# Kernel optimization log

Measured on AMD Instinct MI355X. Metric: run time of the kernel, lower is better.

## Reference

```python
import jax, jax.numpy as jnp
import numpy as np

N_NODES = 100000
N_EDGES = 640000
D = 128
L = 3
NUM_GRAPHS = 128


def setup_inputs() -> dict:
    key = jax.random.key(0)
    ks = jax.random.split(key, 8)
    scale = 1.0 / np.sqrt(D)
    x = jax.random.normal(ks[0], (N_NODES, D), dtype=jnp.float32)
    edge_index = jax.random.randint(ks[1], (2, N_EDGES), 0, N_NODES, dtype=jnp.int64)
    batch = jnp.sort(jax.random.randint(ks[2], (N_NODES,), 0, NUM_GRAPHS, dtype=jnp.int64))
    W1 = jax.random.normal(ks[3], (L, D, D), dtype=jnp.float32) * scale
    b1 = jnp.zeros((L, D), dtype=jnp.float32)
    W2 = jax.random.normal(ks[4], (L, D, D), dtype=jnp.float32) * scale
    b2 = jnp.zeros((L, D), dtype=jnp.float32)
    return {"x": x, "edge_index": edge_index, "batch": batch,
            "W1": W1, "b1": b1, "W2": W2, "b2": b2}


def reference(x, edge_index, batch, W1, b1, W2, b2):
    # GIN forward: per layer z = ReLU(MLP((1+eps)*z + sum_{j in N(i)} z_j)), eps=0
    n = x.shape[0]
    src, dst = edge_index[0], edge_index[1]  # messages flow src -> dst
    z = x
    for l in range(W1.shape[0]):
        agg = jax.ops.segment_sum(z[src], dst, num_segments=n)  # scatter-add aggregation
        h = agg + z                                             # (1+eps)*x_i + sum x_j, eps=0
        h = jnp.maximum(h @ W1[l] + b1[l], 0.0)                 # Linear + ReLU
        z = h @ W2[l] + b2[l]                                   # Linear
        z = jnp.maximum(z, 0.0)                                 # F.relu after conv
    # global mean pool over graph ids (dropout is identity in eval / p=0)
    ones = jnp.ones((n,), dtype=z.dtype)
    counts = jax.ops.segment_sum(ones, batch, num_segments=NUM_GRAPHS)
    sums = jax.ops.segment_sum(z, batch, num_segments=NUM_GRAPHS)
    g = sums / jnp.maximum(counts, 1.0)[:, None]
    return z, g
```

## Files before the change

### kernel.cpp

```cpp
#include <hip/hip_runtime.h>
#include <hip/hip_bf16.h>

#define D 128
#define NG 128

typedef __attribute__((ext_vector_type(8))) short bf16x8;
typedef __attribute__((ext_vector_type(4))) float f32x4;

__device__ inline unsigned short f2bf(float f) {
  union { float f; unsigned u; } c; c.f = f;
  unsigned u = c.u;
  return (unsigned short)((u + 0x7FFFu + ((u >> 16) & 1u)) >> 16);
}
__device__ inline float bf2f(unsigned short b) {
  union { unsigned u; float f; } c; c.u = ((unsigned)b) << 16;
  return c.f;
}

__global__ void prep_w(const float* __restrict__ W1, const float* __restrict__ W2,
                       unsigned short* __restrict__ Wt1, unsigned short* __restrict__ Wt2,
                       int* __restrict__ deg, int N, float* __restrict__ g) {
  int t = blockIdx.x * 256 + threadIdx.x;
  if (t < N) deg[t] = 0;
  if (t < NG * D) g[t] = 0.f;
  if (t >= 3 * 128 * 128) return;
  int l = t >> 14, k = (t >> 7) & 127, n = t & 127;
  int o = (l << 14) + (n << 7) + k;
  Wt1[o] = f2bf(W1[t]);
  Wt2[o] = f2bf(W2[t]);
}


__global__ void hist_deg(const int* __restrict__ dst, int* __restrict__ deg, int E) {
  int e = blockIdx.x * 256 + threadIdx.x;
  if (e < E) atomicAdd(deg + dst[e], 1);
}

__global__ __launch_bounds__(256) void scan1(const int* __restrict__ deg,
    int* __restrict__ rowptr, int* __restrict__ bsum, int n) {
  __shared__ int sh[256];
  int tid = threadIdx.x;
  int idx = blockIdx.x * 1024 + tid * 4;
  int v[4], tsum = 0;
#pragma unroll
  for (int j = 0; j < 4; ++j) { v[j] = (idx + j < n) ? deg[idx + j] : 0; tsum += v[j]; }
  sh[tid] = tsum;
  __syncthreads();
  for (int off = 1; off < 256; off <<= 1) {
    int x = (tid >= off) ? sh[tid - off] : 0;
    __syncthreads();
    sh[tid] += x;
    __syncthreads();
  }
  if (tid == 255) bsum[blockIdx.x] = sh[255];
  int run = sh[tid] - tsum;
#pragma unroll
  for (int j = 0; j < 4; ++j) { if (idx + j < n) rowptr[idx + j] = run; run += v[j]; }
}

__global__ __launch_bounds__(128) void scan2(int* __restrict__ bsum, int nb) {
  __shared__ int sh[128];
  int tid = threadIdx.x;
  int v = (tid < nb) ? bsum[tid] : 0;
  sh[tid] = v;
  __syncthreads();
  for (int off = 1; off < 128; off <<= 1) {
    int x = (tid >= off) ? sh[tid - off] : 0;
    __syncthreads();
    sh[tid] += x;
    __syncthreads();
  }
  if (tid < nb) bsum[tid] = sh[tid] - v;
}

__global__ void scan3(int* __restrict__ rowptr, int* __restrict__ pos,
                      const int* __restrict__ bsum, int n, int E) {
  int t = blockIdx.x * 256 + threadIdx.x;
  if (t < n) {
    int v = rowptr[t] + bsum[t >> 10];
    rowptr[t] = v;
    pos[t] = v;
  }
  if (t == 0) rowptr[n] = E;
}

__global__ void edge_scatter(const int* __restrict__ src, const int* __restrict__ dst,
                             int* __restrict__ pos, int* __restrict__ csr_src, int E) {
  int e = blockIdx.x * 256 + threadIdx.x;
  if (e >= E) return;
  int idx = atomicAdd(pos + dst[e], 1);
  csr_src[idx] = src[e];
}


template<bool IN_BF16>
__global__ __launch_bounds__(256) void gather_agg(const void* __restrict__ zin,
    const int* __restrict__ rowptr, const int* __restrict__ csr_src,
    unsigned short* __restrict__ agg, int N) {
  int t = blockIdx.x * 256 + threadIdx.x;
  int node = t >> 3;
  if (node >= N) return;
  int c = (t & 7) * 16;
  const float* zf = (const float*)zin;
  const unsigned short* zb = (const unsigned short*)zin;

  float acc[16];

  if constexpr (IN_BF16) {
    const unsigned short* p = zb + (size_t)node * D + c;
    bf16x8 v0 = *(const bf16x8*)(p);
    bf16x8 v1 = *(const bf16x8*)(p + 8);
#pragma unroll
    for (int j = 0; j < 8; ++j) {
      acc[j]     = bf2f((unsigned short)v0[j]);
      acc[j + 8] = bf2f((unsigned short)v1[j]);
    }
  } else {
    const float* p = zf + (size_t)node * D + c;
    float4 v0 = *(const float4*)(p);
    float4 v1 = *(const float4*)(p + 4);
    float4 v2 = *(const float4*)(p + 8);
    float4 v3 = *(const float4*)(p + 12);
    acc[0]  = v0.x; acc[1]  = v0.y; acc[2]  = v0.z; acc[3]  = v0.w;
    acc[4]  = v1.x; acc[5]  = v1.y; acc[6]  = v1.z; acc[7]  = v1.w;
    acc[8]  = v2.x; acc[9]  = v2.y; acc[10] = v2.z; acc[11] = v2.w;
    acc[12] = v3.x; acc[13] = v3.y; acc[14] = v3.z; acc[15] = v3.w;
  }

  int e  = rowptr[node];
  int e1 = rowptr[node + 1];

  if constexpr (IN_BF16) {
    for (; e + 4 <= e1; e += 4) {
      int s0 = csr_src[e + 0];
      int s1 = csr_src[e + 1];
      int s2 = csr_src[e + 2];
      int s3 = csr_src[e + 3];
      const unsigned short* p0 = zb + (size_t)s0 * D + c;
      const unsigned short* p1 = zb + (size_t)s1 * D + c;
      const unsigned short* p2 = zb + (size_t)s2 * D + c;
      const unsigned short* p3 = zb + (size_t)s3 * D + c;
      bf16x8 a0 = *(const bf16x8*)(p0), a1 = *(const bf16x8*)(p0 + 8);
      bf16x8 b0 = *(const bf16x8*)(p1), b1 = *(const bf16x8*)(p1 + 8);
      bf16x8 c0 = *(const bf16x8*)(p2), c1 = *(const bf16x8*)(p2 + 8);
      bf16x8 d0 = *(const bf16x8*)(p3), d1 = *(const bf16x8*)(p3 + 8);
#pragma unroll
      for (int j = 0; j < 8; ++j) {
        acc[j]     += (bf2f((unsigned short)a0[j]) + bf2f((unsigned short)b0[j]))
                    + (bf2f((unsigned short)c0[j]) + bf2f((unsigned short)d0[j]));
        acc[j + 8] += (bf2f((unsigned short)a1[j]) + bf2f((unsigned short)b1[j]))
                    + (bf2f((unsigned short)c1[j]) + bf2f((unsigned short)d1[j]));
      }
    }
    if (e + 2 <= e1) {
      int s0 = csr_src[e + 0];
      int s1 = csr_src[e + 1];
      const unsigned short* p0 = zb + (size_t)s0 * D + c;
      const unsigned short* p1 = zb + (size_t)s1 * D + c;
      bf16x8 a0 = *(const bf16x8*)(p0), a1 = *(const bf16x8*)(p0 + 8);
      bf16x8 b0 = *(const bf16x8*)(p1), b1 = *(const bf16x8*)(p1 + 8);
#pragma unroll
      for (int j = 0; j < 8; ++j) {
        acc[j]     += bf2f((unsigned short)a0[j]) + bf2f((unsigned short)b0[j]);
        acc[j + 8] += bf2f((unsigned short)a1[j]) + bf2f((unsigned short)b1[j]);
      }
      e += 2;
    }
    if (e < e1) {
      int s0 = csr_src[e];
      const unsigned short* p0 = zb + (size_t)s0 * D + c;
      bf16x8 a0 = *(const bf16x8*)(p0), a1 = *(const bf16x8*)(p0 + 8);
#pragma unroll
      for (int j = 0; j < 8; ++j) {
        acc[j]     += bf2f((unsigned short)a0[j]);
        acc[j + 8] += bf2f((unsigned short)a1[j]);
      }
    }
  } else {
    for (; e + 2 <= e1; e += 2) {
      int s0 = csr_src[e + 0];
      int s1 = csr_src[e + 1];
      const float* p0 = zf + (size_t)s0 * D + c;
      const float* p1 = zf + (size_t)s1 * D + c;
      float4 u0 = *(const float4*)(p0);
      float4 u1 = *(const float4*)(p0 + 4);
      float4 u2 = *(const float4*)(p0 + 8);
      float4 u3 = *(const float4*)(p0 + 12);
      float4 w0 = *(const float4*)(p1);
      float4 w1 = *(const float4*)(p1 + 4);
      float4 w2 = *(const float4*)(p1 + 8);
      float4 w3 = *(const float4*)(p1 + 12);
      acc[0]  += u0.x + w0.x; acc[1]  += u0.y + w0.y;
      acc[2]  += u0.z + w0.z; acc[3]  += u0.w + w0.w;
      acc[4]  += u1.x + w1.x; acc[5]  += u1.y + w1.y;
      acc[6]  += u1.z + w1.z; acc[7]  += u1.w + w1.w;
      acc[8]  += u2.x + w2.x; acc[9]  += u2.y + w2.y;
      acc[10] += u2.z + w2.z; acc[11] += u2.w + w2.w;
      acc[12] += u3.x + w3.x; acc[13] += u3.y + w3.y;
      acc[14] += u3.z + w3.z; acc[15] += u3.w + w3.w;
    }
    if (e < e1) {
      int s0 = csr_src[e];
      const float* p0 = zf + (size_t)s0 * D + c;
      float4 u0 = *(const float4*)(p0);
      float4 u1 = *(const float4*)(p0 + 4);
      float4 u2 = *(const float4*)(p0 + 8);
      float4 u3 = *(const float4*)(p0 + 12);
      acc[0]  += u0.x; acc[1]  += u0.y; acc[2]  += u0.z; acc[3]  += u0.w;
      acc[4]  += u1.x; acc[5]  += u1.y; acc[6]  += u1.z; acc[7]  += u1.w;
      acc[8]  += u2.x; acc[9]  += u2.y; acc[10] += u2.z; acc[11] += u2.w;
      acc[12] += u3.x; acc[13] += u3.y; acc[14] += u3.z; acc[15] += u3.w;
    }
  }

  bf16x8 o0, o1;
#pragma unroll
  for (int j = 0; j < 8; ++j) {
    o0[j] = (short)f2bf(acc[j]);
    o1[j] = (short)f2bf(acc[j + 8]);
  }
  unsigned short* q = agg + (size_t)node * D + c;
  *(bf16x8*)(q)     = o0;
  *(bf16x8*)(q + 8) = o1;
}


template<bool LAST>
__global__ __launch_bounds__(256, 2) void gemm_fused(const unsigned short* __restrict__ A,
    const unsigned short* __restrict__ Wt1, const float* __restrict__ b1v,
    const unsigned short* __restrict__ Wt2, const float* __restrict__ b2v,
    unsigned short* __restrict__ Zb, float* __restrict__ Zf, int M, int nt) {
  __shared__ unsigned short w2s[128][136];
  __shared__ unsigned short hs[4][16][136];
  int tid  = threadIdx.x;
  int lane = tid & 63;
  int wid  = tid >> 6;
  int c16  = lane & 15;
  int kq   = lane >> 4;
  int koff = kq * 8;

#pragma unroll
  for (int i = 0; i < 8; ++i) {
    int chunk = i * 256 + tid;
    int row = chunk >> 4, k16 = chunk & 15;
    *(bf16x8*)&w2s[row][k16 * 8] = *(const bf16x8*)(Wt2 + (size_t)row * D + k16 * 8);
  }

  bf16x8 bf1[8][4];
  float  bb1[8], bb2[8];
#pragma unroll
  for (int fc = 0; fc < 8; ++fc) {
    int col = fc * 16 + c16;
    bb1[fc] = b1v[col];
    bb2[fc] = b2v[col];
#pragma unroll
    for (int kk = 0; kk < 4; ++kk)
      bf1[fc][kk] = *(const bf16x8*)(Wt1 + (size_t)col * D + kk * 32 + koff);
  }

  int tile0 = blockIdx.x * 2;
  int tile1 = tile0 + 1;

  auto LOADA = [&](bf16x8 (&dst)[2][4], int tile) {
#pragma unroll
    for (int h = 0; h < 2; ++h) {
      int row = tile * 128 + wid * 32 + h * 16 + c16;
      row = row < M ? row : M - 1;
#pragma unroll
      for (int kk = 0; kk < 4; ++kk)
        dst[h][kk] = *(const bf16x8*)(A + (size_t)row * D + kk * 32 + koff);
    }
  };

  bf16x8 aA[2][4], aB[2][4];
  LOADA(aA, tile0);
  __syncthreads();

  auto DO_HALF = [&](const bf16x8 (&a)[4], int rb) {
#pragma unroll
    for (int fc = 0; fc < 8; ++fc) {
      f32x4 acc = {0.f, 0.f, 0.f, 0.f};
#pragma unroll
      for (int kk = 0; kk < 4; ++kk)
        acc = __builtin_amdgcn_mfma_f32_16x16x32_bf16(a[kk], bf1[fc][kk], acc, 0, 0, 0);
      int col = fc * 16 + c16;
#pragma unroll
      for (int r = 0; r < 4; ++r)
        hs[wid][kq * 4 + r][col] = f2bf(fmaxf(acc[r] + bb1[fc], 0.f));
    }
    bf16x8 a2[4];
#pragma unroll
    for (int kk = 0; kk < 4; ++kk)
      a2[kk] = *(const bf16x8*)&hs[wid][c16][kk * 32 + koff];
#pragma unroll
    for (int fc = 0; fc < 8; ++fc) {
      f32x4 acc = {0.f, 0.f, 0.f, 0.f};
      int col = fc * 16 + c16;
#pragma unroll
      for (int kk = 0; kk < 4; ++kk) {
        bf16x8 b = *(const bf16x8*)&w2s[col][kk * 32 + koff];
        acc = __builtin_amdgcn_mfma_f32_16x16x32_bf16(a2[kk], b, acc, 0, 0, 0);
      }
      if constexpr (LAST) {
#pragma unroll
        for (int r = 0; r < 4; ++r) {
          int row = rb + kq * 4 + r;
          if (row < M) Zf[(size_t)row * D + col] = fmaxf(acc[r] + bb2[fc], 0.f);
        }
      } else {
#pragma unroll
        for (int r = 0; r < 4; ++r)
          hs[wid][kq * 4 + r][col] = f2bf(fmaxf(acc[r] + bb2[fc], 0.f));
      }
    }
    if constexpr (!LAST) {
#pragma unroll
      for (int i = 0; i < 4; ++i) {
        int rl = i * 4 + kq;
        bf16x8 v = *(const bf16x8*)&hs[wid][rl][c16 * 8];
        int row = rb + rl;
        if (row < M)
          *(bf16x8*)(Zb + (size_t)row * D + c16 * 8) = v;
      }
    }
  };

  DO_HALF(aA[0], tile0 * 128 + wid * 32);
  if (tile1 < nt) LOADA(aB, tile1);
  DO_HALF(aA[1], tile0 * 128 + wid * 32 + 16);
  if (tile1 < nt) {
    DO_HALF(aB[0], tile1 * 128 + wid * 32);
    DO_HALF(aB[1], tile1 * 128 + wid * 32 + 16);
  }
}


__global__ __launch_bounds__(128) void pool_bounds(const int* __restrict__ batch,
                                                   int* __restrict__ start, int N) {
  int g = threadIdx.x;
  int lo = 0, hi = N;
  while (lo < hi) {
    int mid = (lo + hi) >> 1;
    if (batch[mid] < g) lo = mid + 1; else hi = mid;
  }
  start[g] = lo;
  if (g == 0) start[NG] = N;
}

#define PCHUNKS 8
__global__ __launch_bounds__(128) void pool_mean(const float* __restrict__ z,
    const int* __restrict__ start, float* __restrict__ g) {
  int gid   = blockIdx.x >> 3;
  int chunk = blockIdx.x & (PCHUNKS - 1);
  int col = threadIdx.x;
  int s = start[gid], epos = start[gid + 1];
  int len = epos - s;
  if (len <= 0) return;
  int per = (len + PCHUNKS - 1) / PCHUNKS;
  int r0 = s + chunk * per;
  int r1 = min(r0 + per, epos);
  if (r0 >= r1) return;
  float a0 = 0.f, a1 = 0.f, a2 = 0.f, a3 = 0.f;
  int i = r0;
  for (; i + 4 <= r1; i += 4) {
    a0 += z[(size_t)(i + 0) * D + col];
    a1 += z[(size_t)(i + 1) * D + col];
    a2 += z[(size_t)(i + 2) * D + col];
    a3 += z[(size_t)(i + 3) * D + col];
  }
  for (; i < r1; ++i) a0 += z[(size_t)i * D + col];
  atomicAdd(g + (size_t)gid * D + col, (a0 + a1) + (a2 + a3));
}

__global__ void pool_div(float* __restrict__ g, const int* __restrict__ start) {
  int t = blockIdx.x * 256 + threadIdx.x;
  if (t >= NG * D) return;
  int gid = t >> 7;
  int cnt = start[gid + 1] - start[gid];
  g[t] = g[t] / fmaxf((float)cnt, 1.f);
}

extern "C" void kernel_launch(void* const* d_in, const int* in_sizes, int n_in,
                              void* d_out, int out_size, void* d_ws, size_t ws_size,
                              hipStream_t stream) {
  const float* x     = (const float*)d_in[0];
  const int*   ei    = (const int*)d_in[1];
  const int*   batch = (const int*)d_in[2];
  const float* W1    = (const float*)d_in[3];
  const float* b1    = (const float*)d_in[4];
  const float* W2    = (const float*)d_in[5];
  const float* b2    = (const float*)d_in[6];

  const int N = in_sizes[0] / D;
  const int E = in_sizes[1] / 2;
  const int* src = ei;
  const int* dst = ei + E;

  float* zout = (float*)d_out;
  float* g    = zout + (size_t)N * D;

  char* w = (char*)d_ws;
  unsigned short* agg     = (unsigned short*)w;    w += (size_t)N * D * 2;
  unsigned short* zb      = (unsigned short*)w;    w += (size_t)N * D * 2;
  unsigned short* Wt1     = (unsigned short*)w;    w += 3 * 16384 * 2;
  unsigned short* Wt2     = (unsigned short*)w;    w += 3 * 16384 * 2;
  int*            start   = (int*)w;               w += (NG + 4) * 4;
  int*            deg     = (int*)w;               w += (size_t)N * 4;
  int*            rowptr  = (int*)w;               w += (size_t)(N + 4) * 4;
  int*            pos     = (int*)w;               w += (size_t)N * 4;
  int*            bsum    = (int*)w;               w += 128 * 4;
  int*            csr_src = (int*)w;               w += (size_t)E * 4;

  const int nb = (N + 1023) / 1024;

  int prep_threads = (3 * 128 * 128 > N) ? 3 * 128 * 128 : N;
  prep_w<<<(prep_threads + 255) / 256, 256, 0, stream>>>(W1, W2, Wt1, Wt2, deg, N, g);

  pool_bounds<<<1, 128, 0, stream>>>(batch, start, N);

  hist_deg<<<(E + 255) / 256, 256, 0, stream>>>(dst, deg, E);
  scan1<<<nb, 256, 0, stream>>>(deg, rowptr, bsum, N);
  scan2<<<1, 128, 0, stream>>>(bsum, nb);
  scan3<<<(N + 255) / 256, 256, 0, stream>>>(rowptr, pos, bsum, N, E);
  edge_scatter<<<(E + 255) / 256, 256, 0, stream>>>(src, dst, pos, csr_src, E);

  const int gather_blocks = (int)(((size_t)N * 8 + 255) / 256);
  const int nt            = (N + 127) / 128;
  const int gemm_blocks   = (nt + 1) / 2;

  gather_agg<false><<<gather_blocks, 256, 0, stream>>>(x, rowptr, csr_src, agg, N);
  gemm_fused<false><<<gemm_blocks, 256, 0, stream>>>(agg, Wt1, b1, Wt2, b2, zb, zout, N, nt);
  gather_agg<true><<<gather_blocks, 256, 0, stream>>>(zb, rowptr, csr_src, agg, N);
  gemm_fused<false><<<gemm_blocks, 256, 0, stream>>>(agg, Wt1 + 16384, b1 + 128,
                                                     Wt2 + 16384, b2 + 128, zb, zout, N, nt);
  gather_agg<true><<<gather_blocks, 256, 0, stream>>>(zb, rowptr, csr_src, agg, N);
  gemm_fused<true><<<gemm_blocks, 256, 0, stream>>>(agg, Wt1 + 32768, b1 + 256,
                                                    Wt2 + 32768, b2 + 256, zb, zout, N, nt);

  pool_mean<<<NG * PCHUNKS, 128, 0, stream>>>(zout, start, g);
  pool_div<<<(NG * D + 255) / 256, 256, 0, stream>>>(g, start);
}
```

Baseline: 289.4 us.

## Process two row fragments per MFMA loop in fused GEMM and fold pool_bounds into prep

The fused MLP GEMM now runs a wave's full 32-row slice per pass with two interleaved accumulators. This reuses each weight fragment and LDS read of W2 across both fragments and exposes more independent MFMAs. Both A tiles are loaded up front, before the weight staging, so their latency overlaps it. The pool_bounds binary search moves into prep_w to remove one kernel launch. This doubles the per-wave LDS scratch and raises register pressure, which may hurt the two-blocks-per-CU occupancy target.

```diff
diff --git a/kernel.cpp b/kernel.cpp
--- a/kernel.cpp
+++ b/kernel.cpp
@@ -19,10 +19,20 @@
 
 __global__ void prep_w(const float* __restrict__ W1, const float* __restrict__ W2,
                        unsigned short* __restrict__ Wt1, unsigned short* __restrict__ Wt2,
-                       int* __restrict__ deg, int N, float* __restrict__ g) {
+                       int* __restrict__ deg, int N, float* __restrict__ g,
+                       const int* __restrict__ batch, int* __restrict__ start) {
   int t = blockIdx.x * 256 + threadIdx.x;
   if (t < N) deg[t] = 0;
   if (t < NG * D) g[t] = 0.f;
+  if (t < NG) {
+    int lo = 0, hi = N;
+    while (lo < hi) {
+      int mid = (lo + hi) >> 1;
+      if (batch[mid] < t) lo = mid + 1; else hi = mid;
+    }
+    start[t] = lo;
+    if (t == 0) start[NG] = N;
+  }
   if (t >= 3 * 128 * 128) return;
   int l = t >> 14, k = (t >> 7) & 127, n = t & 127;
   int o = (l << 14) + (n << 7) + k;
@@ -231,7 +241,7 @@
     const unsigned short* __restrict__ Wt2, const float* __restrict__ b2v,
     unsigned short* __restrict__ Zb, float* __restrict__ Zf, int M, int nt) {
   __shared__ unsigned short w2s[128][136];
-  __shared__ unsigned short hs[4][16][136];
+  __shared__ unsigned short hs[4][32][136];
   int tid  = threadIdx.x;
   int lane = tid & 63;
   int wid  = tid >> 6;
@@ -239,6 +249,23 @@
   int kq   = lane >> 4;
   int koff = kq * 8;
 
+  int tile0 = blockIdx.x * 2;
+  int tile1 = tile0 + 1;
+
+  bf16x8 aA[2][4], aB[2][4];
+#pragma unroll
+  for (int h = 0; h < 2; ++h) {
+    int rowA = tile0 * 128 + wid * 32 + h * 16 + c16;
+    rowA = rowA < M ? rowA : M - 1;
+    int rowB = tile1 * 128 + wid * 32 + h * 16 + c16;
+    rowB = rowB < M ? rowB : M - 1;
+#pragma unroll
+    for (int kk = 0; kk < 4; ++kk) {
+      aA[h][kk] = *(const bf16x8*)(A + (size_t)rowA * D + kk * 32 + koff);
+      aB[h][kk] = *(const bf16x8*)(A + (size_t)rowB * D + kk * 32 + koff);
+    }
+  }
+
 #pragma unroll
   for (int i = 0; i < 8; ++i) {
     int chunk = i * 256 + tid;
@@ -258,64 +285,62 @@
       bf1[fc][kk] = *(const bf16x8*)(Wt1 + (size_t)col * D + kk * 32 + koff);
   }
 
-  int tile0 = blockIdx.x * 2;
-  int tile1 = tile0 + 1;
-
-  auto LOADA = [&](bf16x8 (&dst)[2][4], int tile) {
-#pragma unroll
-    for (int h = 0; h < 2; ++h) {
-      int row = tile * 128 + wid * 32 + h * 16 + c16;
-      row = row < M ? row : M - 1;
+  __syncthreads();
+
+  auto TILE = [&](const bf16x8 (&a)[2][4], int tile) {
+    int rb = tile * 128 + wid * 32;
+#pragma unroll
+    for (int fc = 0; fc < 8; ++fc) {
+      f32x4 acc0 = {0.f, 0.f, 0.f, 0.f};
+      f32x4 acc1 = {0.f, 0.f, 0.f, 0.f};
+#pragma unroll
+      for (int kk = 0; kk < 4; ++kk) {
+        acc0 = __builtin_amdgcn_mfma_f32_16x16x32_bf16(a[0][kk], bf1[fc][kk], acc0, 0, 0, 0);
+        acc1 = __builtin_amdgcn_mfma_f32_16x16x32_bf16(a[1][kk], bf1[fc][kk], acc1, 0, 0, 0);
+      }
+      int col = fc * 16 + c16;
+#pragma unroll
+      for (int r = 0; r < 4; ++r) {
+        hs[wid][kq * 4 + r][col]      = f2bf(fmaxf(acc0[r] + bb1[fc], 0.f));
+        hs[wid][kq * 4 + r + 16][col] = f2bf(fmaxf(acc1[r] + bb1[fc], 0.f));
+      }
+    }
+    bf16x8 a2[2][4];
+#pragma unroll
+    for (int fr = 0; fr < 2; ++fr)
 #pragma unroll
       for (int kk = 0; kk < 4; ++kk)
-        dst[h][kk] = *(const bf16x8*)(A + (size_t)row * D + kk * 32 + koff);
-    }
-  };
-
-  bf16x8 aA[2][4], aB[2][4];
-  LOADA(aA, tile0);
-  __syncthreads();
-
-  auto DO_HALF = [&](const bf16x8 (&a)[4], int rb) {
+        a2[fr][kk] = *(const bf16x8*)&hs[wid][fr * 16 + c16][kk * 32 + koff];
 #pragma unroll
     for (int fc = 0; fc < 8; ++fc) {
-      f32x4 acc = {0.f, 0.f, 0.f, 0.f};
-#pragma unroll
-      for (int kk = 0; kk < 4; ++kk)
-        acc = __builtin_amdgcn_mfma_f32_16x16x32_bf16(a[kk], bf1[fc][kk], acc, 0, 0, 0);
-      int col = fc * 16 + c16;
-#pragma unroll
-      for (int r = 0; r < 4; ++r)
-        hs[wid][kq * 4 + r][col] = f2bf(fmaxf(acc[r] + bb1[fc], 0.f));
-    }
-    bf16x8 a2[4];
-#pragma unroll
-    for (int kk = 0; kk < 4; ++kk)
-      a2[kk] = *(const bf16x8*)&hs[wid][c16][kk * 32 + koff];
-#pragma unroll
-    for (int fc = 0; fc < 8; ++fc) {
-      f32x4 acc = {0.f, 0.f, 0.f, 0.f};
+      f32x4 acc0 = {0.f, 0.f, 0.f, 0.f};
+      f32x4 acc1 = {0.f, 0.f, 0.f, 0.f};
       int col = fc * 16 + c16;
 #pragma unroll
       for (int kk = 0; kk < 4; ++kk) {
         bf16x8 b = *(const bf16x8*)&w2s[col][kk * 32 + koff];
-        acc = __builtin_amdgcn_mfma_f32_16x16x32_bf16(a2[kk], b, acc, 0, 0, 0);
+        acc0 = __builtin_amdgcn_mfma_f32_16x16x32_bf16(a2[0][kk], b, acc0, 0, 0, 0);
+        acc1 = __builtin_amdgcn_mfma_f32_16x16x32_bf16(a2[1][kk], b, acc1, 0, 0, 0);
       }
       if constexpr (LAST) {
 #pragma unroll
         for (int r = 0; r < 4; ++r) {
-          int row = rb + kq * 4 + r;
-          if (row < M) Zf[(size_t)row * D + col] = fmaxf(acc[r] + bb2[fc], 0.f);
+          int row0 = rb + kq * 4 + r;
+          if (row0 < M) Zf[(size_t)row0 * D + col] = fmaxf(acc0[r] + bb2[fc], 0.f);
+          int row1 = row0 + 16;
+          if (row1 < M) Zf[(size_t)row1 * D + col] = fmaxf(acc1[r] + bb2[fc], 0.f);
         }
       } else {
 #pragma unroll
-        for (int r = 0; r < 4; ++r)
-          hs[wid][kq * 4 + r][col] = f2bf(fmaxf(acc[r] + bb2[fc], 0.f));
+        for (int r = 0; r < 4; ++r) {
+          hs[wid][kq * 4 + r][col]      = f2bf(fmaxf(acc0[r] + bb2[fc], 0.f));
+          hs[wid][kq * 4 + r + 16][col] = f2bf(fmaxf(acc1[r] + bb2[fc], 0.f));
+        }
       }
     }
     if constexpr (!LAST) {
 #pragma unroll
-      for (int i = 0; i < 4; ++i) {
+      for (int i = 0; i < 8; ++i) {
         int rl = i * 4 + kq;
         bf16x8 v = *(const bf16x8*)&hs[wid][rl][c16 * 8];
         int row = rb + rl;
@@ -325,27 +350,10 @@
     }
   };
 
-  DO_HALF(aA[0], tile0 * 128 + wid * 32);
-  if (tile1 < nt) LOADA(aB, tile1);
-  DO_HALF(aA[1], tile0 * 128 + wid * 32 + 16);
-  if (tile1 < nt) {
-    DO_HALF(aB[0], tile1 * 128 + wid * 32);
-    DO_HALF(aB[1], tile1 * 128 + wid * 32 + 16);
-  }
-}
-
-
-__global__ __launch_bounds__(128) void pool_bounds(const int* __restrict__ batch,
-                                                   int* __restrict__ start, int N) {
-  int g = threadIdx.x;
-  int lo = 0, hi = N;
-  while (lo < hi) {
-    int mid = (lo + hi) >> 1;
-    if (batch[mid] < g) lo = mid + 1; else hi = mid;
-  }
-  start[g] = lo;
-  if (g == 0) start[NG] = N;
-}
+  TILE(aA, tile0);
+  if (tile1 < nt) TILE(aB, tile1);
+}
+
 
 #define PCHUNKS 8
 __global__ __launch_bounds__(128) void pool_mean(const float* __restrict__ z,
@@ -414,9 +422,8 @@
   const int nb = (N + 1023) / 1024;
 
   int prep_threads = (3 * 128 * 128 > N) ? 3 * 128 * 128 : N;
-  prep_w<<<(prep_threads + 255) / 256, 256, 0, stream>>>(W1, W2, Wt1, Wt2, deg, N, g);
-
-  pool_bounds<<<1, 128, 0, stream>>>(batch, start, N);
+  prep_w<<<(prep_threads + 255) / 256, 256, 0, stream>>>(W1, W2, Wt1, Wt2, deg, N, g,
+                                                         batch, start);
 
   hist_deg<<<(E + 255) / 256, 256, 0, stream>>>(dst, deg, E);
   scan1<<<nb, 256, 0, stream>>>(deg, rowptr, bsum, N);
```

After: 279.4 us. 1.04x faster.
